# Kernel tuning notes

Measured on AMD Instinct MI355X. Metric: run time of the kernel, lower is better.

## Reference

```python
import jax, jax.numpy as jnp
import numpy as np

VOCAB_P1 = 100001  # vocab_size + 1
EMB_DIM = 128
BATCH = 256
NNZ_Q = 2048
NNZ_D = 262144


def setup_inputs() -> dict:
    key = jax.random.key(0)
    ks = jax.random.split(key, 10)
    return {
        "q_rows": jax.random.randint(ks[0], (NNZ_Q,), 0, VOCAB_P1, dtype=jnp.int32),
        "q_cols": jax.random.randint(ks[1], (NNZ_Q,), 0, BATCH, dtype=jnp.int32),
        "q_vals": jax.random.uniform(ks[2], (NNZ_Q,), dtype=jnp.float32),
        "d_rows": jax.random.randint(ks[3], (NNZ_D,), 0, VOCAB_P1, dtype=jnp.int32),
        "d_cols": jax.random.randint(ks[4], (NNZ_D,), 0, BATCH, dtype=jnp.int32),
        "d_freqs": jax.random.uniform(ks[5], (NNZ_D,), dtype=jnp.float32),
        "emb": jax.random.normal(ks[6], (VOCAB_P1, EMB_DIM), dtype=jnp.float32) * 0.1,
        "W1": jax.random.normal(ks[7], (EMB_DIM, 100), dtype=jnp.float32) * (2.0 / EMB_DIM) ** 0.5,
        "b1": jnp.zeros((100,), dtype=jnp.float32),
        "W2": jax.random.normal(ks[8], (100, 1), dtype=jnp.float32) * (2.0 / 100) ** 0.5,
        "b2": jnp.ones((1,), dtype=jnp.float32),
        "mu": jnp.float32(2500.0),
        "batch_size": BATCH,
    }


def _scatter_dense(rows, cols, vals, batch_size):
    # tf.sparse.to_dense: dense [vocab+1, batch] with values at (row, col).
    # Indices are (assumed) unique, so add == set; add keeps it a clean scatter.
    return jnp.zeros((VOCAB_P1, batch_size), vals.dtype).at[rows, cols].add(vals)


def reference(q_rows, q_cols, q_vals, d_rows, d_cols, d_freqs,
              emb, W1, b1, W2, b2, mu, batch_size):
    # query bag-of-words dense tensor [V, B]
    q = _scatter_dense(q_rows, q_cols, q_vals, batch_size)

    # term discrimination value MLP on document terms (dropout disabled = eval mode)
    h = jax.nn.relu(emb[d_rows] @ W1 + b1)          # [nnz_d, 100]
    tdv = jax.nn.relu(h @ W2 + b2)[:, 0]            # [nnz_d]
    freq_tdv = tdv * d_freqs                        # [nnz_d]

    # weighted document term-frequency dense tensor [V, B]
    d = _scatter_dense(d_rows, d_cols, freq_tdv, batch_size)

    cfreq = jnp.sum(d, axis=1) / jnp.sum(d)                     # [V]
    smoothing = jnp.log(mu / (jnp.sum(d, axis=0) + mu))         # [B]
    dir_d = jnp.log1p(d / (1.0 + mu * cfreq[:, None])) + smoothing  # [V, B]
    rel = jnp.sum(q * dir_d, axis=0)                            # [B]
    return (rel, d)
```

## Files before the change

kernel.cpp:

```cpp
#include <hip/hip_runtime.h>
#include <stdint.h>

#define VOCAB_P1 100001
#define EMB_DIM  128
#define BATCH    256
#define NNZ_Q    2048
#define NNZ_D    262144

#define NPAD 112
#define ROWP 136
#define NGRP 6251

typedef __attribute__((ext_vector_type(8))) short  short8;
typedef __attribute__((ext_vector_type(4))) float  float4v;

__device__ __forceinline__ unsigned short f2bf(float f) {
    union { float f; unsigned u; } v; v.f = f;
    unsigned u = v.u;
    u += 0x7fffu + ((u >> 16) & 1u);
    return (unsigned short)(u >> 16);
}

__device__ __forceinline__ short8 cvt8(float4 a, float4 b) {
    short8 r;
    r[0] = (short)f2bf(a.x); r[1] = (short)f2bf(a.y);
    r[2] = (short)f2bf(a.z); r[3] = (short)f2bf(a.w);
    r[4] = (short)f2bf(b.x); r[5] = (short)f2bf(b.y);
    r[6] = (short)f2bf(b.z); r[7] = (short)f2bf(b.w);
    return r;
}

__global__ __launch_bounds__(256) void mlp_tdv_kernel(
    const float* __restrict__ emb, const float* __restrict__ W1,
    const float* __restrict__ b1, const float* __restrict__ W2,
    const float* __restrict__ b2, float* __restrict__ tdvtab)
{
    __shared__ __align__(16) short w1t[NPAD * ROWP];
    __shared__ float b1s[NPAD];
    __shared__ float w2s[NPAD];

    const int tid = threadIdx.x;

    int* w1i = (int*)w1t;
    for (int i = tid; i < NPAD * ROWP / 2; i += 256) w1i[i] = 0;
    __syncthreads();
    for (int f = tid; f < EMB_DIM * 100; f += 256) {
        int k = f / 100, j = f - k * 100;
        w1t[j * ROWP + k] = (short)f2bf(W1[f]);
    }
    if (tid < NPAD) {
        b1s[tid] = (tid < 100) ? b1[tid] : 0.f;
        w2s[tid] = (tid < 100) ? W2[tid] : 0.f;
    }
    __syncthreads();

    const int lane = tid & 63;
    const int w    = tid >> 6;
    const int col  = lane & 15;
    const int quad = lane >> 4;
    const float b2v = b2[0];
    const int nw = gridDim.x * 4;

    for (int grp = blockIdx.x * 4 + w; grp < NGRP; grp += nw) {
        int r  = grp * 16 + col;
        int rr = (r <= VOCAB_P1 - 1) ? r : (VOCAB_P1 - 1);
        const float* rp = emb + (size_t)rr * EMB_DIM + quad * 8;
        float4 u0 = *(const float4*)(rp);
        float4 u1 = *(const float4*)(rp + 4);
        float4 u2 = *(const float4*)(rp + 32);
        float4 u3 = *(const float4*)(rp + 36);
        float4 u4 = *(const float4*)(rp + 64);
        float4 u5 = *(const float4*)(rp + 68);
        float4 u6 = *(const float4*)(rp + 96);
        float4 u7 = *(const float4*)(rp + 100);
        short8 a0 = cvt8(u0, u1), a1 = cvt8(u2, u3);
        short8 a2 = cvt8(u4, u5), a3 = cvt8(u6, u7);

        float s0 = 0.f, s1 = 0.f, s2 = 0.f, s3 = 0.f;
        for (int jt = 0; jt < 7; ++jt) {
            const short* bp = &w1t[(jt * 16 + col) * ROWP + quad * 8];
            short8 bv0 = *(const short8*)(bp);
            short8 bv1 = *(const short8*)(bp + 32);
            short8 bv2 = *(const short8*)(bp + 64);
            short8 bv3 = *(const short8*)(bp + 96);

            float4v acc = {0.f, 0.f, 0.f, 0.f};
            acc = __builtin_amdgcn_mfma_f32_16x16x32_bf16(a0, bv0, acc, 0, 0, 0);
            acc = __builtin_amdgcn_mfma_f32_16x16x32_bf16(a1, bv1, acc, 0, 0, 0);
            acc = __builtin_amdgcn_mfma_f32_16x16x32_bf16(a2, bv2, acc, 0, 0, 0);
            acc = __builtin_amdgcn_mfma_f32_16x16x32_bf16(a3, bv3, acc, 0, 0, 0);

            float b1v = b1s[jt * 16 + col];
            float w2v = w2s[jt * 16 + col];
            float h;
            h = acc[0] + b1v; h = h > 0.f ? h : 0.f; s0 += h * w2v;
            h = acc[1] + b1v; h = h > 0.f ? h : 0.f; s1 += h * w2v;
            h = acc[2] + b1v; h = h > 0.f ? h : 0.f; s2 += h * w2v;
            h = acc[3] + b1v; h = h > 0.f ? h : 0.f; s3 += h * w2v;
        }
        for (int m = 1; m < 16; m <<= 1) {
            s0 += __shfl_xor(s0, m, 64);
            s1 += __shfl_xor(s1, m, 64);
            s2 += __shfl_xor(s2, m, 64);
            s3 += __shfl_xor(s3, m, 64);
        }
        if (col < 4) {
            float sv = (col == 0) ? s0 : (col == 1) ? s1 : (col == 2) ? s2 : s3;
            int row = grp * 16 + quad * 4 + col;
            if (row < VOCAB_P1) {
                float tdv = sv + b2v;
                tdvtab[row] = tdv > 0.f ? tdv : 0.f;
            }
        }
    }
}

__global__ __launch_bounds__(256) void scatter_kernel(
    const int* __restrict__ d_rows, const int* __restrict__ d_cols,
    const float* __restrict__ d_freqs, const float* __restrict__ tdvtab,
    float* __restrict__ dmat, float* __restrict__ rowsum,
    float* __restrict__ colsum)
{
    __shared__ float cs[BATCH];
    const int tid = threadIdx.x;
    cs[tid] = 0.f;
    __syncthreads();

    int g = blockIdx.x * 256 + tid;
    int4   r4 = ((const int4*)d_rows)[g];
    int4   c4 = ((const int4*)d_cols)[g];
    float4 f4 = ((const float4*)d_freqs)[g];

    float t0 = tdvtab[r4.x], t1 = tdvtab[r4.y];
    float t2 = tdvtab[r4.z], t3 = tdvtab[r4.w];
    float ft0 = t0 * f4.x, ft1 = t1 * f4.y, ft2 = t2 * f4.z, ft3 = t3 * f4.w;

    atomicAdd(&dmat[(size_t)r4.x * BATCH + c4.x], ft0);
    atomicAdd(&dmat[(size_t)r4.y * BATCH + c4.y], ft1);
    atomicAdd(&dmat[(size_t)r4.z * BATCH + c4.z], ft2);
    atomicAdd(&dmat[(size_t)r4.w * BATCH + c4.w], ft3);
    atomicAdd(&rowsum[r4.x], ft0);
    atomicAdd(&rowsum[r4.y], ft1);
    atomicAdd(&rowsum[r4.z], ft2);
    atomicAdd(&rowsum[r4.w], ft3);
    atomicAdd(&cs[c4.x], ft0);
    atomicAdd(&cs[c4.y], ft1);
    atomicAdd(&cs[c4.z], ft2);
    atomicAdd(&cs[c4.w], ft3);

    __syncthreads();
    atomicAdd(&colsum[tid], cs[tid]);
}

__global__ __launch_bounds__(256) void rel_kernel(
    const int* __restrict__ q_rows, const int* __restrict__ q_cols,
    const float* __restrict__ q_vals, const float* __restrict__ dmat,
    const float* __restrict__ rowsum, const float* __restrict__ colsum,
    const float* __restrict__ mu_p, float* __restrict__ rel)
{
    __shared__ float csh[BATCH];
    __shared__ float red[BATCH];
    const int tid = threadIdx.x;
    float c = colsum[tid];
    csh[tid] = c;
    red[tid] = c;
    __syncthreads();
    for (int s = 128; s > 0; s >>= 1) {
        if (tid < s) red[tid] += red[tid + s];
        __syncthreads();
    }
    float tot = red[0];
    float mu  = mu_p[0];

    int e = blockIdx.x * 256 + tid;
    int v = q_rows[e], b = q_cols[e];
    float dval = dmat[(size_t)v * BATCH + b];
    float cf   = rowsum[v] / tot;
    float dir  = log1pf(dval / (1.f + mu * cf)) + logf(mu / (csh[b] + mu));
    atomicAdd(&rel[b], q_vals[e] * dir);
}

extern "C" void kernel_launch(void* const* d_in, const int* in_sizes, int n_in,
                              void* d_out, int out_size, void* d_ws, size_t ws_size,
                              hipStream_t stream)
{
    const int*   q_rows  = (const int*)d_in[0];
    const int*   q_cols  = (const int*)d_in[1];
    const float* q_vals  = (const float*)d_in[2];
    const int*   d_rows  = (const int*)d_in[3];
    const int*   d_cols  = (const int*)d_in[4];
    const float* d_freqs = (const float*)d_in[5];
    const float* emb     = (const float*)d_in[6];
    const float* W1      = (const float*)d_in[7];
    const float* b1      = (const float*)d_in[8];
    const float* W2      = (const float*)d_in[9];
    const float* b2      = (const float*)d_in[10];
    const float* mu      = (const float*)d_in[11];

    float* rel  = (float*)d_out;
    float* dmat = rel + BATCH;

    float* rowsum = (float*)d_ws;
    float* colsum = rowsum + 100352;
    float* tdvtab = colsum + 256;

    hipMemsetAsync(d_out, 0, (size_t)out_size * sizeof(float), stream);
    hipMemsetAsync(d_ws, 0, (size_t)(100352 + 256) * sizeof(float), stream);

    mlp_tdv_kernel<<<1024, 256, 0, stream>>>(emb, W1, b1, W2, b2, tdvtab);
    scatter_kernel<<<NNZ_D / 1024, 256, 0, stream>>>(
        d_rows, d_cols, d_freqs, tdvtab, dmat, rowsum, colsum);
    rel_kernel<<<NNZ_Q / 256, 256, 0, stream>>>(
        q_rows, q_cols, q_vals, dmat, rowsum, colsum, mu, rel);
}
```

Before: 221.0 us.

## Replace memsets with a single zero kernel and scatter one element per thread

New measurement: 240.9 us. 1.09x slower.

```diff
diff --git a/kernel.cpp b/kernel.cpp
--- a/kernel.cpp
+++ b/kernel.cpp
@@ -10,6 +10,8 @@
 #define NPAD 112
 #define ROWP 136
 #define NGRP 6251
+
+#define WS_ZERO_FLOATS (100352 + 256)
 
 typedef __attribute__((ext_vector_type(8))) short  short8;
 typedef __attribute__((ext_vector_type(4))) float  float4v;
@@ -28,6 +30,17 @@
     r[4] = (short)f2bf(b.x); r[5] = (short)f2bf(b.y);
     r[6] = (short)f2bf(b.z); r[7] = (short)f2bf(b.w);
     return r;
+}
+
+__global__ __launch_bounds__(256) void zero_kernel(
+    float4* __restrict__ a, int n4a, float4* __restrict__ b, int n4b)
+{
+    const float4 z = {0.f, 0.f, 0.f, 0.f};
+    int stride = gridDim.x * 256;
+    for (int i = blockIdx.x * 256 + threadIdx.x; i < n4a; i += stride)
+        a[i] = z;
+    for (int i = blockIdx.x * 256 + threadIdx.x; i < n4b; i += stride)
+        b[i] = z;
 }
 
 __global__ __launch_bounds__(256) void mlp_tdv_kernel(
@@ -126,27 +139,15 @@
     cs[tid] = 0.f;
     __syncthreads();
 
-    int g = blockIdx.x * 256 + tid;
-    int4   r4 = ((const int4*)d_rows)[g];
-    int4   c4 = ((const int4*)d_cols)[g];
-    float4 f4 = ((const float4*)d_freqs)[g];
-
-    float t0 = tdvtab[r4.x], t1 = tdvtab[r4.y];
-    float t2 = tdvtab[r4.z], t3 = tdvtab[r4.w];
-    float ft0 = t0 * f4.x, ft1 = t1 * f4.y, ft2 = t2 * f4.z, ft3 = t3 * f4.w;
-
-    atomicAdd(&dmat[(size_t)r4.x * BATCH + c4.x], ft0);
-    atomicAdd(&dmat[(size_t)r4.y * BATCH + c4.y], ft1);
-    atomicAdd(&dmat[(size_t)r4.z * BATCH + c4.z], ft2);
-    atomicAdd(&dmat[(size_t)r4.w * BATCH + c4.w], ft3);
-    atomicAdd(&rowsum[r4.x], ft0);
-    atomicAdd(&rowsum[r4.y], ft1);
-    atomicAdd(&rowsum[r4.z], ft2);
-    atomicAdd(&rowsum[r4.w], ft3);
-    atomicAdd(&cs[c4.x], ft0);
-    atomicAdd(&cs[c4.y], ft1);
-    atomicAdd(&cs[c4.z], ft2);
-    atomicAdd(&cs[c4.w], ft3);
+    int e = blockIdx.x * 256 + tid;
+    int   r = d_rows[e];
+    int   c = d_cols[e];
+    float f = d_freqs[e];
+    float ft = tdvtab[r] * f;
+
+    atomicAdd(&dmat[(size_t)r * BATCH + c], ft);
+    atomicAdd(&rowsum[r], ft);
+    atomicAdd(&cs[c], ft);
 
     __syncthreads();
     atomicAdd(&colsum[tid], cs[tid]);
@@ -204,11 +205,11 @@
     float* colsum = rowsum + 100352;
     float* tdvtab = colsum + 256;
 
-    hipMemsetAsync(d_out, 0, (size_t)out_size * sizeof(float), stream);
-    hipMemsetAsync(d_ws, 0, (size_t)(100352 + 256) * sizeof(float), stream);
+    zero_kernel<<<2048, 256, 0, stream>>>(
+        (float4*)d_out, out_size / 4, (float4*)d_ws, WS_ZERO_FLOATS / 4);
 
     mlp_tdv_kernel<<<1024, 256, 0, stream>>>(emb, W1, b1, W2, b2, tdvtab);
-    scatter_kernel<<<NNZ_D / 1024, 256, 0, stream>>>(
+    scatter_kernel<<<NNZ_D / 256, 256, 0, stream>>>(
         d_rows, d_cols, d_freqs, tdvtab, dmat, rowsum, colsum);
     rel_kernel<<<NNZ_Q / 256, 256, 0, stream>>>(
         q_rows, q_cols, q_vals, dmat, rowsum, colsum, mu, rel);
```
